# Kernel optimization log

Measured on AMD Instinct MI355X. Metric: run time of the kernel, lower is better.

Reference implementation:

```python
import jax, jax.numpy as jnp
import numpy as np

ANCHORS = np.array([[116., 90.], [156., 198.], [373., 326.],
                    [30., 61.], [62., 45.], [59., 119.],
                    [10., 13.], [16., 30.], [33., 23.]], dtype=np.float32)
IMG_WH = (416.0, 416.0)  # image_size[::-1]
IGNORE_THRESH = 0.5
MAX_BOXES = 64  # static upper bound on true boxes per image per layer


def bce_logits(t, x):
    # tf.nn.sigmoid_cross_entropy_with_logits(labels=t, logits=x)
    return jnp.maximum(x, 0.0) - x * t + jnp.log1p(jnp.exp(-jnp.abs(x)))


def box_iou(b1, b2):
    # b1: [B,H,W,3,4] xywh, b2: [B,M,4] xywh -> iou [B,H,W,3,M]
    b1 = b1[..., None, :]
    b2 = b2[:, None, None, None, :, :]
    b1_min = b1[..., :2] - b1[..., 2:4] * 0.5
    b1_max = b1[..., :2] + b1[..., 2:4] * 0.5
    b2_min = b2[..., :2] - b2[..., 2:4] * 0.5
    b2_max = b2[..., :2] + b2[..., 2:4] * 0.5
    inter_wh = jnp.maximum(jnp.minimum(b1_max, b2_max) - jnp.maximum(b1_min, b2_min), 0.0)
    inter = inter_wh[..., 0] * inter_wh[..., 1]
    a1 = b1[..., 2] * b1[..., 3]
    a2 = b2[..., 2] * b2[..., 3]
    return inter / (a1 + a2 - inter)


def layer_loss(yt, pred, anchors):
    # yt: [B,H,W,3,5+C], pred: [B,H,W,3*(5+C)]
    B, H, W = yt.shape[:3]
    C = pred.shape[-1] // 3 - 5
    p = pred.reshape(B, H, W, 3, 5 + C)
    gy, gx = jnp.meshgrid(jnp.arange(H), jnp.arange(W), indexing='ij')
    grid = jnp.stack([gx, gy], -1).astype(pred.dtype)[:, :, None, :]  # [H,W,1,2]
    fwh = jnp.array([W, H], pred.dtype)
    anc = anchors.reshape(1, 1, 1, 3, 2)
    # pred_process (channel layout: 0=conf, 1:3=xy, 3:5=wh, 5:=class)
    xy = (jax.nn.sigmoid(p[..., 1:3]) + grid) / fwh
    wh = jnp.exp(p[..., 3:5]) * anc / fwh
    conf = jax.nn.sigmoid(p[..., 0:1])
    cls = jax.nn.sigmoid(p[..., 5:])
    pred_box = jnp.concatenate([xy, wh], -1)

    obj = yt[..., 0:1]
    true_cls = yt[..., 5:]
    true_xy = yt[..., 1:3] * fwh - grid
    true_wh = jnp.log(yt[..., 3:5] / anc * jnp.array(IMG_WH, yt.dtype))
    true_wh = jnp.where(obj > 0, true_wh, jnp.zeros_like(true_wh))
    scale = 2.0 - yt[..., 3:4] * yt[..., 4:5]

    # vectorized replacement for the per-image while_loop + boolean_mask:
    # gather the MAX_BOXES highest-objectness cells per image as candidate true boxes
    flat_obj = obj[..., 0].reshape(B, -1)
    flat_box = yt[..., 1:5].reshape(B, -1, 4)
    vals, idx = jax.lax.top_k(flat_obj, MAX_BOXES)
    tboxes = jnp.take_along_axis(flat_box, idx[..., None], axis=1)  # [B,M,4]
    iou = box_iou(pred_box, tboxes)                                 # [B,H,W,3,M]
    iou = jnp.where((vals > 0.5)[:, None, None, None, :], iou, -jnp.inf)
    best_iou = jnp.max(iou, axis=-1)  # -inf when no true boxes (matches tf reduce_max over empty)
    ignore = (best_iou < IGNORE_THRESH).astype(yt.dtype)[..., None]

    xy_l = obj * scale * bce_logits(true_xy, xy)
    wh_l = obj * scale * 0.5 * jnp.square(true_wh - wh)
    conf_l = obj * bce_logits(obj, conf) + (1.0 - obj) * bce_logits(obj, conf) * ignore
    cls_l = obj * bce_logits(true_cls, cls)
    red = lambda t: jnp.sum(t, axis=(1, 2, 3, 4))
    return red(xy_l) + red(wh_l) + red(conf_l) + red(cls_l)


def yolo_loss(y_true, p0, p1, p2):
    B, _, A, D = y_true.shape
    yts = [y_true[:, 0:169].reshape(B, 13, 13, A, D),
           y_true[:, 169:845].reshape(B, 26, 26, A, D),
           y_true[:, 845:3549].reshape(B, 52, 52, A, D)]
    anc = jnp.asarray(ANCHORS)
    total = jnp.zeros((B,), y_true.dtype)
    for i, pred in enumerate([p0, p1, p2]):
        total = total + layer_loss(yts[i], pred, anc[3 * i:3 * i + 3])
    return total


def setup_inputs() -> dict:
    key = jax.random.key(0)
    B, N, C = 32, 3549, 80
    k1, k2, k3, k4, k5, k6, k7 = jax.random.split(key, 7)
    obj = (jax.random.uniform(k1, (B, N, 3, 1)) < 0.002).astype(jnp.float32)
    xy = jax.random.uniform(k2, (B, N, 3, 2), minval=0.05, maxval=0.95)
    wh = jax.random.uniform(k3, (B, N, 3, 2), minval=0.05, maxval=0.4)
    cls = (jax.random.uniform(k4, (B, N, 3, C)) < (1.0 / C)).astype(jnp.float32)
    y_true = jnp.concatenate([obj, xy, wh, cls], axis=-1)
    pred_13 = 0.5 * jax.random.normal(k5, (B, 13, 13, 255), dtype=jnp.float32)
    pred_26 = 0.5 * jax.random.normal(k6, (B, 26, 26, 255), dtype=jnp.float32)
    pred_52 = 0.5 * jax.random.normal(k7, (B, 52, 52, 255), dtype=jnp.float32)
    return {"y_true": y_true, "pred_13": pred_13, "pred_26": pred_26, "pred_52": pred_52}


def reference(y_true, pred_13, pred_26, pred_52):
    return yolo_loss(y_true, pred_13, pred_26, pred_52)
```

## Files before the change

kernel.cpp:

```cpp
#include <hip/hip_runtime.h>

#define MAXB 64
#define CAP 256

__constant__ float c_anc[9][2] = {
    {116.f, 90.f}, {156.f, 198.f}, {373.f, 326.f},
    { 30.f, 61.f}, { 62.f, 45.f}, { 59.f, 119.f},
    { 10.f, 13.f}, { 16.f, 30.f}, { 33.f, 23.f}};

typedef float floatx4 __attribute__((ext_vector_type(4), aligned(4)));

__device__ __forceinline__ float sigm(float x) {
    return __builtin_amdgcn_rcpf(1.f + __expf(-x));
}
__device__ __forceinline__ float bce_f(float t, float x) {
    return fmaxf(x, 0.f) - x * t + __logf(1.f + __expf(-fabsf(x)));
}

__device__ __forceinline__ void map_block(int j, int& l, int& blk, int& S,
                                          int& n0, int& nwords) {
    if (j < 2)       { l = 0; blk = j;      S = 13; n0 = 0;   nwords = 8;   }
    else if (j < 10) { l = 1; blk = j - 2;  S = 26; n0 = 169; nwords = 32;  }
    else             { l = 2; blk = j - 10; S = 52; n0 = 845; nwords = 128; }
}

template <int ITERS>
__device__ __forceinline__ void scan_obj(const float* __restrict__ ybase,
                                         int nCells, int lane, int wv,
                                         unsigned long long* swords) {
    float ov[ITERS];
#pragma unroll
    for (int k = 0; k < ITERS; ++k) {
        int c = (((k << 2) + wv) << 6) + lane;
        ov[k] = (c < nCells) ? ybase[(long long)c * 85] : 0.f;
    }
#pragma unroll
    for (int k = 0; k < ITERS; ++k) {
        unsigned long long m = __ballot(ov[k] > 0.5f);
        if (lane == 0) swords[(k << 2) + wv] = m;
    }
}

__global__ void init_k(float* __restrict__ out) { out[threadIdx.x] = 0.f; }

__global__ __launch_bounds__(256) void loss_k(
    const float* __restrict__ yt,
    const float* __restrict__ p13, const float* __restrict__ p26,
    const float* __restrict__ p52, float* __restrict__ out)
{
    int bid = blockIdx.x, tid = threadIdx.x;
    int b = bid / 42, j = bid - b * 42;
    int l, blk, S, n0, nwords;
    map_block(j, l, blk, S, n0, nwords);
    int nCells = S * S * 3;
    float Sf = (float)S;
    float invS = __builtin_amdgcn_rcpf(Sf);
    const float* ybase = yt + (long long)(b * 3549 + n0) * 255;
    const float* pred  = (l == 0) ? p13 : (l == 1) ? p26 : p52;
    const float* pbase = pred + (long long)b * S * S * 255;
    int lane = tid & 63, wv = tid >> 6;

    int c = blk * 256 + tid;
    bool act = c < nCells;
    int cc = act ? c : 0;
    const float* pcp = pbase + (long long)cc * 85;
    floatx4 v03 = *(const floatx4*)pcp;
    float v4 = pcp[4];

    __shared__ unsigned long long swords[128];
    __shared__ int sidx[CAP];
    __shared__ int sbase2[2];
    __shared__ int stot_s;
    __shared__ float sxmin[MAXB], sxmax[MAXB], symin[MAXB], symax[MAXB], sba[MAXB];

    if (l == 0)      scan_obj<2 >(ybase, nCells, lane, wv, swords);
    else if (l == 1) scan_obj<8 >(ybase, nCells, lane, wv, swords);
    else             scan_obj<32>(ybase, nCells, lane, wv, swords);
    __syncthreads();

    unsigned long long w = 0ULL;
    int pc = 0;
    if (tid < 128) { w = (tid < nwords) ? swords[tid] : 0ULL; pc = __popcll(w); }
    int x = pc;
#pragma unroll
    for (int d = 1; d < 64; d <<= 1) {
        int y = __shfl_up(x, d, 64);
        if (lane >= d) x += y;
    }
    if (tid < 128 && lane == 63) sbase2[wv] = x;
    __syncthreads();
    if (tid == 0) stot_s = sbase2[0] + sbase2[1];
    if (tid < 128) {
        int base = x - pc + (wv ? sbase2[0] : 0);
        unsigned long long ww = w;
        while (ww) {
            int bit = __ffsll((long long)ww) - 1;
            if (base < CAP) sidx[base] = tid * 64 + bit;
            ++base;
            ww &= ww - 1;
        }
    }
    __syncthreads();

    int stot = stot_s;
    int TC = stot < CAP ? stot : CAP;
    int MB = TC < MAXB ? TC : MAXB;
    if (tid < MB) {
        int idx = sidx[tid];
        if (idx >= nCells) idx = nCells - 1;
        const float* yc = ybase + (long long)idx * 85;
        float gx = yc[1], gy = yc[2], gww = yc[3], ghh = yc[4];
        sxmin[tid] = gx - gww * 0.5f; sxmax[tid] = gx + gww * 0.5f;
        symin[tid] = gy - ghh * 0.5f; symax[tid] = gy + ghh * 0.5f;
        sba[tid]   = gww * ghh;
    }
    __syncthreads();

    int p_ = cc / 3, a = cc - p_ * 3;
    int gh = p_ / S, gw = p_ - gh * S;
    float aw = c_anc[l * 3 + a][0], ah = c_anc[l * 3 + a][1];
    float px = (sigm(v03.y) + (float)gw) * invS;
    float py = (sigm(v03.z) + (float)gh) * invS;
    float pw = __expf(v03.w) * aw * invS, ph = __expf(v4) * ah * invS;
    float pxmin = px - pw * 0.5f, pxmax = px + pw * 0.5f;
    float pymin = py - ph * 0.5f, pymax = py + ph * 0.5f;
    float parea = pw * ph;
    bool hit = false;
    for (int i = 0; i < MB; ++i) {
        float iw = fminf(pxmax, sxmax[i]) - fmaxf(pxmin, sxmin[i]);
        float ih = fminf(pymax, symax[i]) - fmaxf(pymin, symin[i]);
        float inter = fmaxf(iw, 0.f) * fmaxf(ih, 0.f);
        hit = hit || (3.f * inter >= parea + sba[i]);
    }
    bool posbit = (swords[cc >> 6] >> (cc & 63)) & 1ULL;
    float conf = sigm(v03.x);
    float bval = fmaxf(conf, 0.f) + __logf(1.f + __expf(-fabsf(conf)));
    float loss = (act && !posbit && !hit) ? bval : 0.f;

    if (blk == 0) {
        float wsum = 0.f;
        for (int i = wv; i < TC; i += 4) {
            int idx = sidx[i];
            if (idx >= nCells) idx = nCells - 1;
            const float* yc = ybase + (long long)idx * 85;
            const float* pp = pbase + (long long)idx * 85;
            float part = bce_f(yc[5 + lane], sigm(pp[5 + lane]));
            if (lane < 16)
                part += bce_f(yc[69 + lane], sigm(pp[69 + lane]));
            if (lane == 0) {
                int q = idx / 3, aa = idx - q * 3;
                int qh = q / S, qw = q - qh * S;
                float aw2 = c_anc[l * 3 + aa][0], ah2 = c_anc[l * 3 + aa][1];
                float t1 = yc[1], t2 = yc[2], t3 = yc[3], t4 = yc[4];
                float u0 = pp[0], u1 = pp[1], u2 = pp[2], u3 = pp[3], u4 = pp[4];
                part += bce_f(1.f, sigm(u0));
                float sc = 2.f - t3 * t4;
                float qx = (sigm(u1) + (float)qw) * invS;
                float qy = (sigm(u2) + (float)qh) * invS;
                part += sc * (bce_f(t1 * Sf - (float)qw, qx) +
                              bce_f(t2 * Sf - (float)qh, qy));
                float qpw = __expf(u3) * aw2 * invS;
                float qph = __expf(u4) * ah2 * invS;
                float twx = __logf(t3 / aw2 * 416.f);
                float twy = __logf(t4 / ah2 * 416.f);
                part += sc * 0.5f *
                        ((twx - qpw) * (twx - qpw) + (twy - qph) * (twy - qph));
            }
#pragma unroll
            for (int off = 32; off > 0; off >>= 1)
                part += __shfl_down(part, off, 64);
            if (lane == 0) wsum += part;
        }
        if (lane == 0) loss += wsum;
    }

#pragma unroll
    for (int off = 32; off > 0; off >>= 1)
        loss += __shfl_down(loss, off, 64);
    __shared__ float wred[4];
    if (lane == 0) wred[wv] = loss;
    __syncthreads();
    if (tid == 0)
        atomicAdd(out + b, wred[0] + wred[1] + wred[2] + wred[3]);
}

extern "C" void kernel_launch(void* const* d_in, const int* in_sizes, int n_in,
                              void* d_out, int out_size, void* d_ws, size_t ws_size,
                              hipStream_t stream) {
    (void)in_sizes; (void)n_in; (void)out_size; (void)d_ws; (void)ws_size;
    const float* yt  = (const float*)d_in[0];
    const float* p13 = (const float*)d_in[1];
    const float* p26 = (const float*)d_in[2];
    const float* p52 = (const float*)d_in[3];
    float* out = (float*)d_out;

    init_k<<<1, 32, 0, stream>>>(out);
    loss_k<<<32 * 42, 256, 0, stream>>>(yt, p13, p26, p52, out);
}
```

Measured before the change: 265.2 us.

## Use fewer larger blocks per batch to cut redundant objectness scans

Reorganizes the grid from 42 blocks of 256 threads per batch to 6 blocks of 1024 threads, each thread processing two prediction cells. This reduces how many times each block redundantly scans the objectness column and gathers true boxes for its layer. In exchange the grid shrinks to 192 blocks, which may leave compute units idle and reduce latency hiding.

```diff
diff --git a/kernel.cpp b/kernel.cpp
--- a/kernel.cpp
+++ b/kernel.cpp
@@ -2,6 +2,7 @@
 
 #define MAXB 64
 #define CAP 256
+#define BLK_PER_BATCH 6
 
 __constant__ float c_anc[9][2] = {
     {116.f, 90.f}, {156.f, 198.f}, {373.f, 326.f},
@@ -17,41 +18,38 @@
     return fmaxf(x, 0.f) - x * t + __logf(1.f + __expf(-fabsf(x)));
 }
 
-__device__ __forceinline__ void map_block(int j, int& l, int& blk, int& S,
-                                          int& n0, int& nwords) {
-    if (j < 2)       { l = 0; blk = j;      S = 13; n0 = 0;   nwords = 8;   }
-    else if (j < 10) { l = 1; blk = j - 2;  S = 26; n0 = 169; nwords = 32;  }
-    else             { l = 2; blk = j - 10; S = 52; n0 = 845; nwords = 128; }
-}
+__global__ void init_k(float* __restrict__ out) { out[threadIdx.x] = 0.f; }
 
 template <int ITERS>
 __device__ __forceinline__ void scan_obj(const float* __restrict__ ybase,
-                                         int nCells, int lane, int wv,
-                                         unsigned long long* swords) {
+                                         int nCells, int nwords, int lane,
+                                         int wv, unsigned long long* swords) {
     float ov[ITERS];
 #pragma unroll
     for (int k = 0; k < ITERS; ++k) {
-        int c = (((k << 2) + wv) << 6) + lane;
-        ov[k] = (c < nCells) ? ybase[(long long)c * 85] : 0.f;
+        int wi = k * 16 + wv;
+        int c = (wi << 6) + lane;
+        ov[k] = (wi < nwords && c < nCells) ? ybase[(long long)c * 85] : 0.f;
     }
 #pragma unroll
     for (int k = 0; k < ITERS; ++k) {
+        int wi = k * 16 + wv;
         unsigned long long m = __ballot(ov[k] > 0.5f);
-        if (lane == 0) swords[(k << 2) + wv] = m;
-    }
-}
-
-__global__ void init_k(float* __restrict__ out) { out[threadIdx.x] = 0.f; }
-
-__global__ __launch_bounds__(256) void loss_k(
+        if (lane == 0 && wi < nwords) swords[wi] = m;
+    }
+}
+
+__global__ __launch_bounds__(1024) void loss_k(
     const float* __restrict__ yt,
     const float* __restrict__ p13, const float* __restrict__ p26,
     const float* __restrict__ p52, float* __restrict__ out)
 {
     int bid = blockIdx.x, tid = threadIdx.x;
-    int b = bid / 42, j = bid - b * 42;
-    int l, blk, S, n0, nwords;
-    map_block(j, l, blk, S, n0, nwords);
+    int b = bid / BLK_PER_BATCH, j = bid - b * BLK_PER_BATCH;
+    int l, blk, S, n0, nwords, start, cnt;
+    if (j == 0)      { l = 0; blk = 0;     S = 13; n0 = 0;   nwords = 8;   start = 0;              cnt = 507;  }
+    else if (j == 1) { l = 1; blk = 0;     S = 26; n0 = 169; nwords = 32;  start = 0;              cnt = 2028; }
+    else             { l = 2; blk = j - 2; S = 52; n0 = 845; nwords = 128; start = (j - 2) * 2028; cnt = 2028; }
     int nCells = S * S * 3;
     float Sf = (float)S;
     float invS = __builtin_amdgcn_rcpf(Sf);
@@ -60,12 +58,17 @@
     const float* pbase = pred + (long long)b * S * S * 255;
     int lane = tid & 63, wv = tid >> 6;
 
-    int c = blk * 256 + tid;
-    bool act = c < nCells;
-    int cc = act ? c : 0;
-    const float* pcp = pbase + (long long)cc * 85;
-    floatx4 v03 = *(const floatx4*)pcp;
-    float v4 = pcp[4];
+    int c0 = start + tid;
+    int c1 = start + tid + 1024;
+    bool act0 = (tid < cnt) && (c0 < nCells);
+    bool act1 = (tid + 1024 < cnt) && (c1 < nCells);
+    int cc0 = act0 ? c0 : 0, cc1 = act1 ? c1 : 0;
+    const float* pp0 = pbase + (long long)cc0 * 85;
+    const float* pp1 = pbase + (long long)cc1 * 85;
+    floatx4 v03_0 = *(const floatx4*)pp0;
+    float v4_0 = pp0[4];
+    floatx4 v03_1 = *(const floatx4*)pp1;
+    float v4_1 = pp1[4];
 
     __shared__ unsigned long long swords[128];
     __shared__ int sidx[CAP];
@@ -73,9 +76,9 @@
     __shared__ int stot_s;
     __shared__ float sxmin[MAXB], sxmax[MAXB], symin[MAXB], symax[MAXB], sba[MAXB];
 
-    if (l == 0)      scan_obj<2 >(ybase, nCells, lane, wv, swords);
-    else if (l == 1) scan_obj<8 >(ybase, nCells, lane, wv, swords);
-    else             scan_obj<32>(ybase, nCells, lane, wv, swords);
+    if (l == 0)      scan_obj<1>(ybase, nCells, nwords, lane, wv, swords);
+    else if (l == 1) scan_obj<2>(ybase, nCells, nwords, lane, wv, swords);
+    else             scan_obj<8>(ybase, nCells, nwords, lane, wv, swords);
     __syncthreads();
 
     unsigned long long w = 0ULL;
@@ -116,30 +119,39 @@
     }
     __syncthreads();
 
-    int p_ = cc / 3, a = cc - p_ * 3;
-    int gh = p_ / S, gw = p_ - gh * S;
-    float aw = c_anc[l * 3 + a][0], ah = c_anc[l * 3 + a][1];
-    float px = (sigm(v03.y) + (float)gw) * invS;
-    float py = (sigm(v03.z) + (float)gh) * invS;
-    float pw = __expf(v03.w) * aw * invS, ph = __expf(v4) * ah * invS;
-    float pxmin = px - pw * 0.5f, pxmax = px + pw * 0.5f;
-    float pymin = py - ph * 0.5f, pymax = py + ph * 0.5f;
-    float parea = pw * ph;
-    bool hit = false;
-    for (int i = 0; i < MB; ++i) {
-        float iw = fminf(pxmax, sxmax[i]) - fmaxf(pxmin, sxmin[i]);
-        float ih = fminf(pymax, symax[i]) - fmaxf(pymin, symin[i]);
-        float inter = fmaxf(iw, 0.f) * fmaxf(ih, 0.f);
-        hit = hit || (3.f * inter >= parea + sba[i]);
-    }
-    bool posbit = (swords[cc >> 6] >> (cc & 63)) & 1ULL;
-    float conf = sigm(v03.x);
-    float bval = fmaxf(conf, 0.f) + __logf(1.f + __expf(-fabsf(conf)));
-    float loss = (act && !posbit && !hit) ? bval : 0.f;
+    float loss = 0.f;
+#pragma unroll
+    for (int it = 0; it < 2; ++it) {
+        int cc = it ? cc1 : cc0;
+        bool act = it ? act1 : act0;
+        floatx4 v03 = it ? v03_1 : v03_0;
+        float v4 = it ? v4_1 : v4_0;
+
+        int p_ = cc / 3, a = cc - p_ * 3;
+        int gh = p_ / S, gw = p_ - gh * S;
+        float aw = c_anc[l * 3 + a][0], ah = c_anc[l * 3 + a][1];
+        float px = (sigm(v03.y) + (float)gw) * invS;
+        float py = (sigm(v03.z) + (float)gh) * invS;
+        float pw = __expf(v03.w) * aw * invS, ph = __expf(v4) * ah * invS;
+        float pxmin = px - pw * 0.5f, pxmax = px + pw * 0.5f;
+        float pymin = py - ph * 0.5f, pymax = py + ph * 0.5f;
+        float parea = pw * ph;
+        bool hit = false;
+        for (int i = 0; i < MB; ++i) {
+            float iw = fminf(pxmax, sxmax[i]) - fmaxf(pxmin, sxmin[i]);
+            float ih = fminf(pymax, symax[i]) - fmaxf(pymin, symin[i]);
+            float inter = fmaxf(iw, 0.f) * fmaxf(ih, 0.f);
+            hit = hit || (3.f * inter >= parea + sba[i]);
+        }
+        bool posbit = (swords[cc >> 6] >> (cc & 63)) & 1ULL;
+        float conf = sigm(v03.x);
+        float bval = fmaxf(conf, 0.f) + __logf(1.f + __expf(-fabsf(conf)));
+        loss += (act && !posbit && !hit) ? bval : 0.f;
+    }
 
     if (blk == 0) {
         float wsum = 0.f;
-        for (int i = wv; i < TC; i += 4) {
+        for (int i = wv; i < TC; i += 16) {
             int idx = sidx[i];
             if (idx >= nCells) idx = nCells - 1;
             const float* yc = ybase + (long long)idx * 85;
@@ -177,11 +189,15 @@
 #pragma unroll
     for (int off = 32; off > 0; off >>= 1)
         loss += __shfl_down(loss, off, 64);
-    __shared__ float wred[4];
+    __shared__ float wred[16];
     if (lane == 0) wred[wv] = loss;
     __syncthreads();
-    if (tid == 0)
-        atomicAdd(out + b, wred[0] + wred[1] + wred[2] + wred[3]);
+    if (tid == 0) {
+        float s = 0.f;
+#pragma unroll
+        for (int k = 0; k < 16; ++k) s += wred[k];
+        atomicAdd(out + b, s);
+    }
 }
 
 extern "C" void kernel_launch(void* const* d_in, const int* in_sizes, int n_in,
@@ -195,5 +211,5 @@
     float* out = (float*)d_out;
 
     init_k<<<1, 32, 0, stream>>>(out);
-    loss_k<<<32 * 42, 256, 0, stream>>>(yt, p13, p26, p52, out);
-}
+    loss_k<<<32 * BLK_PER_BATCH, 1024, 0, stream>>>(yt, p13, p26, p52, out);
+}
```

Result: faster. 236.1 us (-11.0%).
